# Kernel optimization log

Hardware: AMD Instinct MI355X
Metric: run time of the kernel (lower is better)

Reference implementation:

```python
import jax, jax.numpy as jnp
import numpy as np

N_NODES = 50000
NFEAT = 512
NHID = 128
N_EDGES = 800000
LN_EPS = 1e-5


def setup_inputs() -> dict:
    key = jax.random.key(0)
    k1, k2, k3, k4, k5 = jax.random.split(key, 5)
    h = jax.random.normal(k1, (N_NODES, NFEAT), dtype=jnp.float32)
    src = jax.random.randint(k2, (N_EDGES,), 0, N_NODES, dtype=jnp.int32)
    dst = jax.random.randint(k3, (N_EDGES,), 0, N_NODES, dtype=jnp.int32)
    # GraphConv params (glorot-ish) + bias; LayerNorm affine params
    W = jax.random.normal(k4, (NFEAT, NHID), dtype=jnp.float32) / np.sqrt(NFEAT)
    b = jnp.zeros((NHID,), dtype=jnp.float32)
    gamma = jnp.ones((NHID,), dtype=jnp.float32)
    beta = jnp.zeros((NHID,), dtype=jnp.float32)
    return {"h": h, "src": src, "dst": dst, "W": W, "b": b, "gamma": gamma, "beta": beta}


def reference(h, src, dst, W, b, gamma, beta):
    n = h.shape[0]
    ones = jnp.ones_like(src, dtype=jnp.float32)
    out_deg = jax.ops.segment_sum(ones, src, num_segments=n)
    in_deg = jax.ops.segment_sum(ones, dst, num_segments=n)
    out_norm = jnp.maximum(out_deg, 1.0) ** -0.5  # [N]
    in_norm = jnp.maximum(in_deg, 1.0) ** -0.5    # [N]

    # norm='both': scale source features by out_deg^{-1/2}
    x = h * out_norm[:, None]
    # in_feats > out_feats -> DGL multiplies by W before aggregation
    x = x @ W  # [N, NHID]
    # sparse aggregate: sum messages over incoming edges
    agg = jax.ops.segment_sum(x[src], dst, num_segments=n)  # [N, NHID]
    agg = agg * in_norm[:, None] + b

    # LayerNorm over last dim
    mu = jnp.mean(agg, axis=-1, keepdims=True)
    var = jnp.mean((agg - mu) ** 2, axis=-1, keepdims=True)
    y = (agg - mu) * jax.lax.rsqrt(var + LN_EPS) * gamma + beta
    return y
```

## Files before the change

kernel.cpp:

```cpp
#include <hip/hip_runtime.h>

#define N_NODES 50000
#define NFEAT   512
#define NHID    128
#define N_EDGES 800000
#define LN_EPS  1e-5f

#define GEMM_ROWS   32
#define GEMM_BLOCKS ((N_NODES + GEMM_ROWS - 1) / GEMM_ROWS)
#define NB_SCAN     ((N_NODES + 1023) / 1024)
#define ZROW        N_NODES

typedef __attribute__((ext_vector_type(8))) short bf16x8;
typedef __attribute__((ext_vector_type(4))) float fx4;

__device__ __forceinline__ unsigned short f2bf(float f) {
    union { float f; unsigned u; } v; v.f = f;
    unsigned r = v.u + 0x7FFF + ((v.u >> 16) & 1);
    return (unsigned short)(r >> 16);
}

__device__ __forceinline__ void bf2x(unsigned u, float& lo, float& hi) {
    union { unsigned u; float f; } a, b;
    a.u = u << 16;
    b.u = u & 0xFFFF0000u;
    lo = a.f; hi = b.f;
}

__global__ __launch_bounds__(256) void prep_kernel(
    const float* __restrict__ W, unsigned short* __restrict__ wf,
    int4* __restrict__ zero_ptr, unsigned short* __restrict__ x)
{
    int t = blockIdx.x * 256 + threadIdx.x;
#pragma unroll
    for (int i = t; i < 25088; i += 16384)
        zero_ptr[i] = make_int4(0, 0, 0, 0);

    if (blockIdx.x == 63 && threadIdx.x < 16)
        ((int4*)(x + (size_t)ZROW * NHID))[threadIdx.x] = make_int4(0, 0, 0, 0);

    if (blockIdx.x < 32) {
        int lane = t & 63;
        int frag = t >> 6;
        int kc = frag >> 3, tt = frag & 7;
        int n  = tt * 16 + (lane & 15);
        int k0 = kc * 32 + (lane >> 4) * 8;
        unsigned short v[8];
#pragma unroll
        for (int j = 0; j < 8; j++)
            v[j] = f2bf(W[(size_t)(k0 + j) * NHID + n]);
        *(bf16x8*)(wf + (size_t)t * 8) = *(bf16x8*)v;
    }
}

__global__ __launch_bounds__(256) void degree_kernel(
    const int* __restrict__ src, const int* __restrict__ dst,
    int* __restrict__ out_deg, int* __restrict__ in_deg,
    int* __restrict__ edge_pos)
{
    int t = blockIdx.x * 256 + threadIdx.x;
    if (t >= N_EDGES / 4) return;
    int4 s4 = ((const int4*)src)[t];
    int4 d4 = ((const int4*)dst)[t];
    int p0 = atomicAdd(&in_deg[d4.x], 1);
    int p1 = atomicAdd(&in_deg[d4.y], 1);
    int p2 = atomicAdd(&in_deg[d4.z], 1);
    int p3 = atomicAdd(&in_deg[d4.w], 1);
    atomicAdd(&out_deg[s4.x], 1);
    atomicAdd(&out_deg[s4.y], 1);
    atomicAdd(&out_deg[s4.z], 1);
    atomicAdd(&out_deg[s4.w], 1);
    ((int4*)edge_pos)[t] = make_int4(p0, p1, p2, p3);
}

__global__ __launch_bounds__(1024) void scan_local(
    const int* __restrict__ in_deg, int* __restrict__ row_ptr, int* __restrict__ bsum,
    const int* __restrict__ out_deg, float* __restrict__ out_norm)
{
    __shared__ int wsum[16];
    const int tid = threadIdx.x;
    const int lane = tid & 63, wave = tid >> 6;
    int i = blockIdx.x * 1024 + tid;
    int v = (i < N_NODES) ? in_deg[i] : 0;
    int sv = v;
#pragma unroll
    for (int off = 1; off < 64; off <<= 1) {
        int t = __shfl_up(sv, off);
        if (lane >= off) sv += t;
    }
    if (lane == 63) wsum[wave] = sv;
    if (i < N_NODES)
        out_norm[i] = rsqrtf(fmaxf((float)out_deg[i], 1.0f));
    __syncthreads();
    if (wave == 0) {
        int wv = (lane < 16) ? wsum[lane] : 0;
#pragma unroll
        for (int off = 1; off < 16; off <<= 1) {
            int t = __shfl_up(wv, off);
            if (lane >= off) wv += t;
        }
        if (lane < 16) wsum[lane] = wv;
    }
    __syncthreads();
    int excl = ((wave > 0) ? wsum[wave - 1] : 0) + (sv - v);
    if (i < N_NODES) row_ptr[i] = excl;
    if (tid == 1023) bsum[blockIdx.x] = wsum[15];
}

__global__ __launch_bounds__(1024) void scan_add2(
    int* __restrict__ row_ptr, const int* __restrict__ bsum)
{
    __shared__ int off_s, tot_s;
    const int tid = threadIdx.x;
    if (tid < 64) {
        int v = (tid < NB_SCAN) ? bsum[tid] : 0;
        int sv = v;
#pragma unroll
        for (int off = 1; off < 64; off <<= 1) {
            int t = __shfl_up(sv, off);
            if (tid >= off) sv += t;
        }
        int pre = __shfl(sv, (blockIdx.x == 0) ? 0 : (blockIdx.x - 1));
        int tot = __shfl(sv, NB_SCAN - 1);
        if (tid == 0) {
            off_s = (blockIdx.x == 0) ? 0 : pre;
            tot_s = tot;
        }
    }
    __syncthreads();
    int i = blockIdx.x * 1024 + tid;
    if (i < N_NODES) row_ptr[i] += off_s;
    if (blockIdx.x == 0 && tid == 0) row_ptr[N_NODES] = tot_s;
}

__global__ __launch_bounds__(256) void fill_kernel(
    const int* __restrict__ src, const int* __restrict__ dst,
    const int* __restrict__ row_ptr, const int* __restrict__ edge_pos,
    int* __restrict__ csr_src)
{
    int e = blockIdx.x * 256 + threadIdx.x;
    if (e < N_EDGES) {
        int d = dst[e];
        csr_src[row_ptr[d] + edge_pos[e]] = src[e];
    }
}

__global__ __launch_bounds__(256) void gemm_kernel(
    const float* __restrict__ h, const unsigned short* __restrict__ wf,
    const float* __restrict__ out_norm, unsigned short* __restrict__ x)
{
    __shared__ __align__(16) unsigned short afrag_lds[2][16 * 64 * 8];
    __shared__ float on_s[32];

    const int tid  = threadIdx.x;
    const int row0 = blockIdx.x * GEMM_ROWS;

    if (tid < 32) {
        int gr = row0 + tid;
        if (gr > N_NODES - 1) gr = N_NODES - 1;
        on_s[tid] = out_norm[gr];
    }

    {
        float4 v[16];
#pragma unroll
        for (int it = 0; it < 16; it++) {
            int i = tid + it * 256;
            int r = i >> 7;
            int grow = row0 + r;
            if (grow > N_NODES - 1) grow = N_NODES - 1;
            v[it] = ((const float4*)h)[(size_t)grow * 128 + (i & 127)];
        }
#pragma unroll
        for (int it = 0; it < 16; it++) {
            int i = tid + it * 256;
            int r  = i >> 7;
            int g  = r >> 4;
            int rr = r & 15;
            int k0 = (i & 127) << 2;
            int kc = k0 >> 5;
            int q  = (k0 >> 3) & 3;
            int j  = k0 & 7;
            int gp = q * 16 + (rr ^ (q | ((kc & 1) << 2)));
            unsigned long long pk =
                (unsigned long long)f2bf(v[it].x)
              | ((unsigned long long)f2bf(v[it].y) << 16)
              | ((unsigned long long)f2bf(v[it].z) << 32)
              | ((unsigned long long)f2bf(v[it].w) << 48);
            *(unsigned long long*)(&afrag_lds[g][0] + kc * 512 + gp * 8 + j) = pk;
        }
    }
    __syncthreads();

    const int wave = tid >> 6;
    const int lane = tid & 63;
    const int t0   = wave * 2;
    const int rr_l = lane & 15;
    const int q_l  = lane >> 4;
    const int g_e  = q_l * 16 + (rr_l ^ q_l);
    const int g_o  = q_l * 16 + (rr_l ^ q_l ^ 4);

    fx4 acc00 = (fx4){0.f, 0.f, 0.f, 0.f};
    fx4 acc01 = (fx4){0.f, 0.f, 0.f, 0.f};
    fx4 acc10 = (fx4){0.f, 0.f, 0.f, 0.f};
    fx4 acc11 = (fx4){0.f, 0.f, 0.f, 0.f};

    const bf16x8* a0p = (const bf16x8*)&afrag_lds[0][0];
    const bf16x8* a1p = (const bf16x8*)&afrag_lds[1][0];
    const bf16x8* wfp = (const bf16x8*)wf + t0 * 64 + lane;

#pragma unroll 4
    for (int kc = 0; kc < 16; kc++) {
        int gidx = (kc & 1) ? g_o : g_e;
        bf16x8 a0 = a0p[kc * 64 + gidx];
        bf16x8 a1 = a1p[kc * 64 + gidx];
        bf16x8 b0 = wfp[kc * 512];
        bf16x8 b1 = wfp[kc * 512 + 64];
        acc00 = __builtin_amdgcn_mfma_f32_16x16x32_bf16(a0, b0, acc00, 0, 0, 0);
        acc01 = __builtin_amdgcn_mfma_f32_16x16x32_bf16(a0, b1, acc01, 0, 0, 0);
        acc10 = __builtin_amdgcn_mfma_f32_16x16x32_bf16(a1, b0, acc10, 0, 0, 0);
        acc11 = __builtin_amdgcn_mfma_f32_16x16x32_bf16(a1, b1, acc11, 0, 0, 0);
    }

    __syncthreads();
    unsigned short* orow = (unsigned short*)&afrag_lds[0][0];
    {
        const int q = lane >> 4;
        const int c = lane & 15;
#pragma unroll
        for (int reg = 0; reg < 4; reg++) {
            int r0 = q * 4 + reg;
            float w0 = on_s[r0];
            float w1 = on_s[16 + r0];
            orow[r0 * 128 + t0 * 16 + c]              = f2bf(acc00[reg] * w0);
            orow[r0 * 128 + (t0 + 1) * 16 + c]        = f2bf(acc01[reg] * w0);
            orow[(16 + r0) * 128 + t0 * 16 + c]       = f2bf(acc10[reg] * w1);
            orow[(16 + r0) * 128 + (t0 + 1) * 16 + c] = f2bf(acc11[reg] * w1);
        }
    }
    __syncthreads();
    {
        const int4* osrc = (const int4*)&afrag_lds[0][0];
#pragma unroll
        for (int p = 0; p < 2; p++) {
            int idx = tid + p * 256;
            int r   = idx >> 4;
            int gr  = row0 + r;
            if (gr < N_NODES)
                ((int4*)x)[(size_t)gr * 16 + (idx & 15)] = osrc[idx];
        }
    }
}

#define ACC4(uu) {                                                        \
    float p0,p1,p2,p3,p4,p5,p6,p7;                                        \
    bf2x(uu.x,p0,p1); bf2x(uu.y,p2,p3);                                   \
    bf2x(uu.z,p4,p5); bf2x(uu.w,p6,p7);                                   \
    a0 += p0; a1 += p1; a2 += p2; a3 += p3;                               \
    a4 += p4; a5 += p5; a6 += p6; a7 += p7; }

__global__ __launch_bounds__(256) void aggregate_kernel(
    const unsigned short* __restrict__ x, const int* __restrict__ row_ptr,
    const int* __restrict__ csr_src,
    const float* __restrict__ b, const float* __restrict__ gamma,
    const float* __restrict__ beta, float* __restrict__ out)
{
    const int n    = blockIdx.x * 4 + (threadIdx.x >> 6);
    const int lane = threadIdx.x & 63;
    const int qi   = lane >> 4;
    const int c    = lane & 15;
    const int start = row_ptr[n];
    const int end   = row_ptr[n + 1];

    float a0 = 0.f, a1 = 0.f, a2 = 0.f, a3 = 0.f;
    float a4 = 0.f, a5 = 0.f, a6 = 0.f, a7 = 0.f;

    for (int base = start; base < end; base += 64) {
        int  me   = base + lane;
        int  msrc = (me < end) ? csr_src[me] : (int)ZROW;
        int cnt = min(64, end - base);
        int ng  = (cnt + 3) >> 2;
        int g = 0;
        for (; g + 4 <= ng; g += 4) {
            int i0 = 4 * g + qi, i1 = i0 + 4, i2 = i0 + 8, i3 = i0 + 12;
            int s0 = __shfl(msrc, i0);
            int s1 = __shfl(msrc, i1);
            int s2 = __shfl(msrc, i2);
            int s3 = __shfl(msrc, i3);
            uint4 u0 = *(const uint4*)(x + (size_t)s0 * NHID + c * 8);
            uint4 u1 = *(const uint4*)(x + (size_t)s1 * NHID + c * 8);
            uint4 u2 = *(const uint4*)(x + (size_t)s2 * NHID + c * 8);
            uint4 u3 = *(const uint4*)(x + (size_t)s3 * NHID + c * 8);
            ACC4(u0) ACC4(u1) ACC4(u2) ACC4(u3)
        }
        for (; g < ng; ++g) {
            int i0 = 4 * g + qi;
            int s0 = __shfl(msrc, i0);
            uint4 u0 = *(const uint4*)(x + (size_t)s0 * NHID + c * 8);
            ACC4(u0)
        }
    }

    a0 += __shfl_xor(a0, 16); a0 += __shfl_xor(a0, 32);
    a1 += __shfl_xor(a1, 16); a1 += __shfl_xor(a1, 32);
    a2 += __shfl_xor(a2, 16); a2 += __shfl_xor(a2, 32);
    a3 += __shfl_xor(a3, 16); a3 += __shfl_xor(a3, 32);
    a4 += __shfl_xor(a4, 16); a4 += __shfl_xor(a4, 32);
    a5 += __shfl_xor(a5, 16); a5 += __shfl_xor(a5, 32);
    a6 += __shfl_xor(a6, 16); a6 += __shfl_xor(a6, 32);
    a7 += __shfl_xor(a7, 16); a7 += __shfl_xor(a7, 32);

    float inorm = rsqrtf(fmaxf((float)(end - start), 1.0f));
    float4 b0 = *(const float4*)(b + c * 8);
    float4 b1 = *(const float4*)(b + c * 8 + 4);
    float v0 = a0 * inorm + b0.x;
    float v1 = a1 * inorm + b0.y;
    float v2 = a2 * inorm + b0.z;
    float v3 = a3 * inorm + b0.w;
    float v4 = a4 * inorm + b1.x;
    float v5 = a5 * inorm + b1.y;
    float v6 = a6 * inorm + b1.z;
    float v7 = a7 * inorm + b1.w;

    float s = ((v0 + v1) + (v2 + v3)) + ((v4 + v5) + (v6 + v7));
#pragma unroll
    for (int off = 8; off > 0; off >>= 1) s += __shfl_xor(s, off);
    float mu = s * (1.0f / 128.0f);

    float d0 = v0 - mu, d1 = v1 - mu, d2 = v2 - mu, d3 = v3 - mu;
    float d4 = v4 - mu, d5 = v5 - mu, d6 = v6 - mu, d7 = v7 - mu;
    float qd = ((d0*d0 + d1*d1) + (d2*d2 + d3*d3)) + ((d4*d4 + d5*d5) + (d6*d6 + d7*d7));
#pragma unroll
    for (int off = 8; off > 0; off >>= 1) qd += __shfl_xor(qd, off);
    float var = qd * (1.0f / 128.0f);
    float rs = rsqrtf(var + LN_EPS);

    if (lane < 16) {
        float4 gg = *(const float4*)(gamma + c * 8);
        float4 be = *(const float4*)(beta + c * 8);
        float4 o;
        o.x = d0 * rs * gg.x + be.x;
        o.y = d1 * rs * gg.y + be.y;
        o.z = d2 * rs * gg.z + be.z;
        o.w = d3 * rs * gg.w + be.w;
        *(float4*)(out + (size_t)n * NHID + c * 8) = o;
    } else if (lane < 32) {
        float4 gg = *(const float4*)(gamma + c * 8 + 4);
        float4 be = *(const float4*)(beta + c * 8 + 4);
        float4 o;
        o.x = d4 * rs * gg.x + be.x;
        o.y = d5 * rs * gg.y + be.y;
        o.z = d6 * rs * gg.z + be.z;
        o.w = d7 * rs * gg.w + be.w;
        *(float4*)(out + (size_t)n * NHID + c * 8 + 4) = o;
    }
}

extern "C" void kernel_launch(void* const* d_in, const int* in_sizes, int n_in,
                              void* d_out, int out_size, void* d_ws, size_t ws_size,
                              hipStream_t stream) {
    const float* h     = (const float*)d_in[0];
    const int*   src   = (const int*)d_in[1];
    const int*   dst   = (const int*)d_in[2];
    const float* W     = (const float*)d_in[3];
    const float* b     = (const float*)d_in[4];
    const float* gamma = (const float*)d_in[5];
    const float* beta  = (const float*)d_in[6];
    float* out = (float*)d_out;

    char* ws = (char*)d_ws;
    const size_t DEG_BYTES = 200704;
    const size_t RP_BYTES  = 200960;
    int*            out_deg  = (int*)(ws);
    int*            in_deg   = (int*)(ws + DEG_BYTES);
    int*            row_ptr  = (int*)(ws + 2 * DEG_BYTES);
    float*          out_norm = (float*)(ws + 2 * DEG_BYTES + RP_BYTES);
    int*            bsum     = (int*)(ws + 3 * DEG_BYTES + RP_BYTES);
    int*            edge_pos = (int*)(ws + 3 * DEG_BYTES + RP_BYTES + 1024);
    int*            csr_src  = (int*)(ws + 3 * DEG_BYTES + RP_BYTES + 1024 + (size_t)N_EDGES * 4);
    unsigned short* wf       = (unsigned short*)(ws + 3 * DEG_BYTES + RP_BYTES + 1024 + 2 * (size_t)N_EDGES * 4);
    unsigned short* x        = (unsigned short*)(ws + 3 * DEG_BYTES + RP_BYTES + 1024 + 2 * (size_t)N_EDGES * 4 + 131072);

    prep_kernel<<<64, 256, 0, stream>>>(W, wf, (int4*)ws, x);
    degree_kernel<<<(N_EDGES / 4 + 255) / 256, 256, 0, stream>>>(
        src, dst, out_deg, in_deg, edge_pos);
    scan_local<<<NB_SCAN, 1024, 0, stream>>>(in_deg, row_ptr, bsum, out_deg, out_norm);
    scan_add2 <<<NB_SCAN, 1024, 0, stream>>>(row_ptr, bsum);
    fill_kernel<<<(N_EDGES + 255) / 256, 256, 0, stream>>>(src, dst, row_ptr, edge_pos, csr_src);
    gemm_kernel<<<GEMM_BLOCKS, 256, 0, stream>>>(h, wf, out_norm, x);
    aggregate_kernel<<<N_NODES / 4, 256, 0, stream>>>(
        x, row_ptr, csr_src, b, gamma, beta, out);
}
```

Before: 296.9 us.

## Replace global-atomic degree counting with per-block LDS 16-bit histograms

After: 283.9 us. 4.4% less time.

```diff
diff --git a/kernel.cpp b/kernel.cpp
--- a/kernel.cpp
+++ b/kernel.cpp
@@ -11,6 +11,12 @@
 #define NB_SCAN     ((N_NODES + 1023) / 1024)
 #define ZROW        N_NODES
 
+#define TBL     50176
+#define NCH_IN  50
+#define EC_IN   16000
+#define NCH_OUT 32
+#define EC_OUT  25000
+
 typedef __attribute__((ext_vector_type(8))) short bf16x8;
 typedef __attribute__((ext_vector_type(4))) float fx4;
 
@@ -29,59 +35,85 @@
 
 __global__ __launch_bounds__(256) void prep_kernel(
     const float* __restrict__ W, unsigned short* __restrict__ wf,
-    int4* __restrict__ zero_ptr, unsigned short* __restrict__ x)
-{
+    unsigned short* __restrict__ x)
+{
+    if (blockIdx.x == 32) {
+        if (threadIdx.x < 16)
+            ((int4*)(x + (size_t)ZROW * NHID))[threadIdx.x] = make_int4(0, 0, 0, 0);
+        return;
+    }
     int t = blockIdx.x * 256 + threadIdx.x;
-#pragma unroll
-    for (int i = t; i < 25088; i += 16384)
-        zero_ptr[i] = make_int4(0, 0, 0, 0);
-
-    if (blockIdx.x == 63 && threadIdx.x < 16)
-        ((int4*)(x + (size_t)ZROW * NHID))[threadIdx.x] = make_int4(0, 0, 0, 0);
-
-    if (blockIdx.x < 32) {
-        int lane = t & 63;
-        int frag = t >> 6;
-        int kc = frag >> 3, tt = frag & 7;
-        int n  = tt * 16 + (lane & 15);
-        int k0 = kc * 32 + (lane >> 4) * 8;
-        unsigned short v[8];
-#pragma unroll
-        for (int j = 0; j < 8; j++)
-            v[j] = f2bf(W[(size_t)(k0 + j) * NHID + n]);
-        *(bf16x8*)(wf + (size_t)t * 8) = *(bf16x8*)v;
-    }
-}
-
-__global__ __launch_bounds__(256) void degree_kernel(
+    int lane = t & 63;
+    int frag = t >> 6;
+    int kc = frag >> 3, tt = frag & 7;
+    int n  = tt * 16 + (lane & 15);
+    int k0 = kc * 32 + (lane >> 4) * 8;
+    unsigned short v[8];
+#pragma unroll
+    for (int j = 0; j < 8; j++)
+        v[j] = f2bf(W[(size_t)(k0 + j) * NHID + n]);
+    *(bf16x8*)(wf + (size_t)t * 8) = *(bf16x8*)v;
+}
+
+__global__ __launch_bounds__(256) void hist_kernel(
     const int* __restrict__ src, const int* __restrict__ dst,
-    int* __restrict__ out_deg, int* __restrict__ in_deg,
-    int* __restrict__ edge_pos)
-{
-    int t = blockIdx.x * 256 + threadIdx.x;
-    if (t >= N_EDGES / 4) return;
-    int4 s4 = ((const int4*)src)[t];
-    int4 d4 = ((const int4*)dst)[t];
-    int p0 = atomicAdd(&in_deg[d4.x], 1);
-    int p1 = atomicAdd(&in_deg[d4.y], 1);
-    int p2 = atomicAdd(&in_deg[d4.z], 1);
-    int p3 = atomicAdd(&in_deg[d4.w], 1);
-    atomicAdd(&out_deg[s4.x], 1);
-    atomicAdd(&out_deg[s4.y], 1);
-    atomicAdd(&out_deg[s4.z], 1);
-    atomicAdd(&out_deg[s4.w], 1);
-    ((int4*)edge_pos)[t] = make_int4(p0, p1, p2, p3);
+    unsigned short* __restrict__ in16, unsigned short* __restrict__ out16,
+    unsigned short* __restrict__ rank16)
+{
+    __shared__ unsigned int hist[TBL / 2];
+    const int tid = threadIdx.x;
+    const int b   = blockIdx.x;
+
+    for (int i = tid; i < TBL / 2; i += 256) hist[i] = 0;
+    __syncthreads();
+
+    if (b < NCH_IN) {
+        const int base = b * EC_IN;
+        for (int i = tid; i < EC_IN; i += 256) {
+            int e = base + i;
+            int d = dst[e];
+            unsigned sh  = (d & 1) * 16;
+            unsigned old = atomicAdd(&hist[d >> 1], 1u << sh);
+            rank16[e] = (unsigned short)((old >> sh) & 0xFFFFu);
+        }
+        __syncthreads();
+        unsigned int* g = (unsigned int*)(in16 + (size_t)b * TBL);
+        for (int i = tid; i < TBL / 2; i += 256) g[i] = hist[i];
+    } else {
+        const int base = (b - NCH_IN) * EC_OUT;
+        for (int i = tid; i < EC_OUT; i += 256) {
+            int s = src[base + i];
+            atomicAdd(&hist[s >> 1], 1u << ((s & 1) * 16));
+        }
+        __syncthreads();
+        unsigned int* g = (unsigned int*)(out16 + (size_t)(b - NCH_IN) * TBL);
+        for (int i = tid; i < TBL / 2; i += 256) g[i] = hist[i];
+    }
 }
 
 __global__ __launch_bounds__(1024) void scan_local(
-    const int* __restrict__ in_deg, int* __restrict__ row_ptr, int* __restrict__ bsum,
-    const int* __restrict__ out_deg, float* __restrict__ out_norm)
+    unsigned short* __restrict__ in16, const unsigned short* __restrict__ out16,
+    int* __restrict__ row_ptr, int* __restrict__ bsum, float* __restrict__ out_norm)
 {
     __shared__ int wsum[16];
     const int tid = threadIdx.x;
     const int lane = tid & 63, wave = tid >> 6;
     int i = blockIdx.x * 1024 + tid;
-    int v = (i < N_NODES) ? in_deg[i] : 0;
+    int v = 0;
+    if (i < N_NODES) {
+        int acc = 0;
+        for (int c = 0; c < NCH_IN; c++) {
+            size_t idx = (size_t)c * TBL + i;
+            int cnt = in16[idx];
+            in16[idx] = (unsigned short)acc;
+            acc += cnt;
+        }
+        v = acc;
+        int od = 0;
+        for (int c = 0; c < NCH_OUT; c++)
+            od += out16[(size_t)c * TBL + i];
+        out_norm[i] = rsqrtf(fmaxf((float)od, 1.0f));
+    }
     int sv = v;
 #pragma unroll
     for (int off = 1; off < 64; off <<= 1) {
@@ -89,8 +121,6 @@
         if (lane >= off) sv += t;
     }
     if (lane == 63) wsum[wave] = sv;
-    if (i < N_NODES)
-        out_norm[i] = rsqrtf(fmaxf((float)out_deg[i], 1.0f));
     __syncthreads();
     if (wave == 0) {
         int wv = (lane < 16) ? wsum[lane] : 0;
@@ -135,13 +165,15 @@
 
 __global__ __launch_bounds__(256) void fill_kernel(
     const int* __restrict__ src, const int* __restrict__ dst,
-    const int* __restrict__ row_ptr, const int* __restrict__ edge_pos,
-    int* __restrict__ csr_src)
+    const int* __restrict__ row_ptr, const unsigned short* __restrict__ in16,
+    const unsigned short* __restrict__ rank16, int* __restrict__ csr_src)
 {
     int e = blockIdx.x * 256 + threadIdx.x;
     if (e < N_EDGES) {
         int d = dst[e];
-        csr_src[row_ptr[d] + edge_pos[e]] = src[e];
+        int c = e / EC_IN;
+        int pos = (int)in16[(size_t)c * TBL + d] + (int)rank16[e];
+        csr_src[row_ptr[d] + pos] = src[e];
     }
 }
 
@@ -368,25 +400,22 @@
     const float* beta  = (const float*)d_in[6];
     float* out = (float*)d_out;
 
-    char* ws = (char*)d_ws;
-    const size_t DEG_BYTES = 200704;
-    const size_t RP_BYTES  = 200960;
-    int*            out_deg  = (int*)(ws);
-    int*            in_deg   = (int*)(ws + DEG_BYTES);
-    int*            row_ptr  = (int*)(ws + 2 * DEG_BYTES);
-    float*          out_norm = (float*)(ws + 2 * DEG_BYTES + RP_BYTES);
-    int*            bsum     = (int*)(ws + 3 * DEG_BYTES + RP_BYTES);
-    int*            edge_pos = (int*)(ws + 3 * DEG_BYTES + RP_BYTES + 1024);
-    int*            csr_src  = (int*)(ws + 3 * DEG_BYTES + RP_BYTES + 1024 + (size_t)N_EDGES * 4);
-    unsigned short* wf       = (unsigned short*)(ws + 3 * DEG_BYTES + RP_BYTES + 1024 + 2 * (size_t)N_EDGES * 4);
-    unsigned short* x        = (unsigned short*)(ws + 3 * DEG_BYTES + RP_BYTES + 1024 + 2 * (size_t)N_EDGES * 4 + 131072);
-
-    prep_kernel<<<64, 256, 0, stream>>>(W, wf, (int4*)ws, x);
-    degree_kernel<<<(N_EDGES / 4 + 255) / 256, 256, 0, stream>>>(
-        src, dst, out_deg, in_deg, edge_pos);
-    scan_local<<<NB_SCAN, 1024, 0, stream>>>(in_deg, row_ptr, bsum, out_deg, out_norm);
+    char* p = (char*)d_ws;
+    unsigned short* in16   = (unsigned short*)p;  p += (size_t)NCH_IN  * TBL * 2;
+    unsigned short* out16  = (unsigned short*)p;
+    int*            csr_src= (int*)p;             p += (size_t)NCH_OUT * TBL * 2;
+    unsigned short* rank16 = (unsigned short*)p;  p += 1600512;
+    int*            row_ptr= (int*)p;             p += 200960;
+    float*          out_norm=(float*)p;           p += 200704;
+    int*            bsum   = (int*)p;             p += 1024;
+    unsigned short* wf     = (unsigned short*)p;  p += 131072;
+    unsigned short* x      = (unsigned short*)p;
+
+    prep_kernel<<<33, 256, 0, stream>>>(W, wf, x);
+    hist_kernel<<<NCH_IN + NCH_OUT, 256, 0, stream>>>(src, dst, in16, out16, rank16);
+    scan_local<<<NB_SCAN, 1024, 0, stream>>>(in16, out16, row_ptr, bsum, out_norm);
     scan_add2 <<<NB_SCAN, 1024, 0, stream>>>(row_ptr, bsum);
-    fill_kernel<<<(N_EDGES + 255) / 256, 256, 0, stream>>>(src, dst, row_ptr, edge_pos, csr_src);
+    fill_kernel<<<(N_EDGES + 255) / 256, 256, 0, stream>>>(src, dst, row_ptr, in16, rank16, csr_src);
     gemm_kernel<<<GEMM_BLOCKS, 256, 0, stream>>>(h, wf, out_norm, x);
     aggregate_kernel<<<N_NODES / 4, 256, 0, stream>>>(
         x, row_ptr, csr_src, b, gamma, beta, out);
```
